# Performance work log

Measured on AMD Instinct MI355X. Metric: run time of the kernel, lower is better.

Reference implementation:

```python
import jax, jax.numpy as jnp
import numpy as np

TAPS = 5
DELAY = 3
ITERATIONS = 2
EPS = 1e-10


def _wpe_one_iteration(Y, power):
    # Y: (B, F, C, T) complex64, power: (B, F, T) float32
    B, F, C, T = Y.shape
    inv_p = 1.0 / jnp.clip(power, EPS)
    Tq = T - DELAY - TAPS + 1  # number of valid frames
    # signal_framing(Y, TAPS, 1)[..., :Tq, :] then reverse last dim:
    # Y_tilde[..., t, k] = Y[..., t + TAPS - 1 - k]  -> (B, F, C, Tq, TAPS)
    Y_tilde = jnp.stack(
        [Y[..., TAPS - 1 - k: TAPS - 1 - k + Tq] for k in range(TAPS)], axis=-1)
    Y_tilde_ip = Y_tilde * inv_p[..., None, DELAY + TAPS - 1:, None]
    # correlation matrix (B, F, taps*C, taps*C)
    R = jnp.einsum('bfdtk,bfetl->bfkdle', jnp.conj(Y_tilde_ip), Y_tilde)
    R = R.reshape(B, F, TAPS * C, TAPS * C)
    # correlation vector (B, F, taps, C, C): indices (k, e, d)
    P = jnp.einsum('bfdtk,bfet->bfked', jnp.conj(Y_tilde_ip),
                   Y[..., DELAY + TAPS - 1:])
    # regularize and invert (batched small complex systems)
    R = R + EPS * jnp.eye(TAPS * C, dtype=R.dtype)
    inv_R = jnp.linalg.inv(R)
    # (B,F,k,e,d) -> (B,F,e,k,d) -> (B,F,C,taps*C)
    vec = jnp.transpose(P, (0, 1, 3, 2, 4)).reshape(B, F, C, TAPS * C)
    # stacked = vec @ inv_R^T  -> (B, F, C, taps*C)
    stacked = jnp.einsum('bfck,bflk->bfcl', vec, inv_R)
    # (B,F,C1,taps,C2) -> filter_matrix_conj (B,F,taps,C2,C1)
    G_conj = jnp.transpose(stacked.reshape(B, F, C, TAPS, C), (0, 1, 3, 4, 2))
    # delayed copies of Y: Y_shift[..., p, :, t] = Y[..., t - DELAY - p] (zero-padded)
    Y_shift = jnp.stack(
        [jnp.pad(Y[..., :T - DELAY - p], [(0, 0)] * 3 + [(DELAY + p, 0)])
         for p in range(TAPS)], axis=-3)  # (B, F, taps, C, T)
    reverb_tail = jnp.einsum('bfpde,bfpdt->bfet', G_conj, Y_shift)
    return Y - reverb_tail


def setup_inputs() -> dict:
    key = jax.random.key(0)
    k1, k2, k3 = jax.random.split(key, 3)
    B, T, C, F = 8, 600, 8, 257
    data_real = jax.random.normal(k1, (B, T, C, F), dtype=jnp.float32)
    data_imag = jax.random.normal(k2, (B, T, C, F), dtype=jnp.float32)
    ilens = jax.random.randint(k3, (B,), 300, T + 1)
    return {"data_real": data_real, "data_imag": data_imag, "ilens": ilens}


def reference(data_real, data_imag, ilens):
    # data: (B, T, C, F) -> (B, F, C, T)
    Y = jax.lax.complex(data_real, data_imag)
    Y = jnp.transpose(Y, (0, 3, 2, 1))
    B, F, C, T = Y.shape
    # use_dnn_mask=False: power averaged over channels -> (B, F, T)
    power = (Y.real ** 2 + Y.imag ** 2).mean(axis=-2)
    enhanced = Y
    for i in range(ITERATIONS):
        if i > 0:
            power = (enhanced.real ** 2 + enhanced.imag ** 2).mean(axis=-2)
        enhanced = _wpe_one_iteration(Y, power)
    # zero out padded frames (make_pad_mask along T)
    tmask = (jnp.arange(T) < ilens[:, None]).astype(enhanced.real.dtype)
    enhanced = enhanced * tmask[:, None, None, :]
    # back to (B, T, C, F)
    enhanced = jnp.transpose(enhanced, (0, 3, 2, 1))
    return enhanced.real, enhanced.imag
```

## Files before the change

### kernel.cpp

```cpp
#include <hip/hip_runtime.h>
#include <hip/hip_bf16.h>

#define Bb 8
#define Tt 600
#define Cc 8
#define Ff 257
#define TAPS 5
#define DELAY 3
#define KC 40
#define NC 48
#define TQ 593
#define TP 602
#define EPSF 1e-10f
#define NTOT (Bb*Tt*Cc*Ff)

__device__ __forceinline__ float2 cmul2(float2 a, float2 b) {
  return make_float2(a.x*b.x - a.y*b.y, a.x*b.y + a.y*b.x);
}

#define CMAC(acc, ax, ay, b)                    \
  acc.x = fmaf(ax, b.x, acc.x);                 \
  acc.x = fmaf(ay, b.y, acc.x);                 \
  acc.y = fmaf(ax, b.y, acc.y);                 \
  acc.y = fmaf(-(ay), b.x, acc.y);

__global__ __launch_bounds__(256) void k_tin(const float* __restrict__ in_re,
                                             const float* __restrict__ in_im,
                                             float2* __restrict__ Yt) {
  __shared__ float2 tile[32][33];
  int f0 = blockIdx.x * 32, t0 = blockIdx.y * 32;
  int b = blockIdx.z >> 3, c = blockIdx.z & 7;
  int tx = threadIdx.x & 31, ty = threadIdx.x >> 5;
#pragma unroll
  for (int ii = 0; ii < 4; ++ii) {
    int t = t0 + ty + 8 * ii, f = f0 + tx;
    if (t < Tt && f < Ff) {
      size_t idx = (((size_t)b * Tt + t) * Cc + c) * Ff + f;
      tile[ty + 8 * ii][tx] = make_float2(in_re[idx], in_im[idx]);
    }
  }
  __syncthreads();
#pragma unroll
  for (int ii = 0; ii < 4; ++ii) {
    int f = f0 + ty + 8 * ii, t = t0 + tx;
    if (f < Ff && t < Tt) {
      size_t o = (((size_t)b * Ff + f) * Cc + c) * Tt + t;
      Yt[o] = tile[tx][ty + 8 * ii];
    }
  }
}

__global__ __launch_bounds__(512, 4) void k_wpe(const float2* __restrict__ Yt,
                                                float2* __restrict__ enh,
                                                const float* __restrict__ in_re,
                                                const float* __restrict__ in_im,
                                                const int* __restrict__ ilens,
                                                float* __restrict__ out_re,
                                                float* __restrict__ out_im,
                                                int load_direct, int store_direct) {
  __shared__ float2 Yl[Cc][TP];
  __shared__ float2 RP[KC][NC + 1];
  __shared__ float wl[Tt];

  int bf = blockIdx.x;
  int b = bf / Ff, f = bf % Ff;
  int tid = threadIdx.x;
  int half = tid >> 8;
  int stid = tid & 255;
  int ty = stid >> 4, tx = stid & 15;

  if (!load_direct) {
    const float4* Yg = (const float4*)(Yt + (size_t)bf * (Cc * Tt));
    for (int i = tid; i < Cc * Tt / 2; i += 512) {
      float4 v = Yg[i];
      int c = i / (Tt / 2), t2 = (i % (Tt / 2)) * 2;
      *(float4*)&Yl[c][t2] = v;
    }
  } else {
    for (int i = tid; i < Cc * Tt; i += 512) {
      int c = i / Tt, t = i % Tt;
      size_t idx = (((size_t)b * Tt + t) * Cc + c) * Ff + f;
      Yl[c][t] = make_float2(in_re[idx], in_im[idx]);
    }
  }
  __syncthreads();

  const float2* YlF = &Yl[0][0];

  bool rv2 = (ty < 8);
  int roff[3];
#pragma unroll
  for (int a = 0; a < 3; ++a) {
    int r = ty + 16 * a;
    if (a == 2 && !rv2) r = 0;
    int k = r >> 3, d = r & 7;
    roff[a] = d * TP + 4 - k;
  }
  int coff[3];
#pragma unroll
  for (int bb = 0; bb < 3; ++bb) {
    int cc = tx + 16 * bb;
    if (cc < KC) { int k = cc >> 3, d = cc & 7; coff[bb] = d * TP + 4 - k; }
    else         { int e = cc - KC;             coff[bb] = e * TP + 7; }
  }

  int tA = half ? 297 : 0;
  int tB = half ? TQ : 297;

  for (int iter = 0; iter < 3; ++iter) {
    if (iter == 0) {
      for (int t = tid; t < Tt; t += 512) {
        float s = 0.f;
#pragma unroll
        for (int c = 0; c < Cc; ++c) { float2 y = Yl[c][t]; s += y.x*y.x + y.y*y.y; }
        wl[t] = 1.0f / fmaxf(s * 0.125f, EPSF);
      }
    } else {
      for (int t = tid; t < Tt; t += 512) {
        float2 acc[Cc];
#pragma unroll
        for (int e = 0; e < Cc; ++e) acc[e] = Yl[e][t];
        for (int p = 0; p < TAPS; ++p) {
          int ts = t - DELAY - p;
          if (ts < 0) break;
#pragma unroll
          for (int d = 0; d < Cc; ++d) {
            float2 u = Yl[d][ts];
            int j = p * Cc + d;
#pragma unroll
            for (int e = 0; e < Cc; ++e) {
              float2 g = RP[j][KC + e];
              acc[e].x -= g.x*u.x - g.y*u.y;
              acc[e].y -= g.x*u.y + g.y*u.x;
            }
          }
        }
        if (iter == 1) {
          float s = 0.f;
#pragma unroll
          for (int e = 0; e < Cc; ++e) s += acc[e].x*acc[e].x + acc[e].y*acc[e].y;
          wl[t] = 1.0f / fmaxf(s * 0.125f, EPSF);
        } else {
          if (!store_direct) {
            float2* Eg = enh + (size_t)bf * (Cc * Tt);
#pragma unroll
            for (int e = 0; e < Cc; ++e) Eg[e * Tt + t] = acc[e];
          } else {
            int il = ilens[b];
            bool live = (t < il);
#pragma unroll
            for (int e = 0; e < Cc; ++e) {
              float2 v = live ? acc[e] : make_float2(0.f, 0.f);
              size_t idx = (((size_t)b * Tt + t) * Cc + e) * Ff + f;
              out_re[idx] = v.x;
              out_im[idx] = v.y;
            }
          }
        }
      }
    }
    if (iter == 2) break;
    __syncthreads();

    float2 racc[3][3];
#pragma unroll
    for (int a = 0; a < 3; ++a)
#pragma unroll
      for (int bb = 0; bb < 3; ++bb) racc[a][bb] = make_float2(0.f, 0.f);

#pragma unroll 2
    for (int t = tA; t < tB; ++t) {
      float w = wl[t + DELAY + TAPS - 1];
      float2 bv0 = YlF[coff[0] + t];
      float2 bv1 = YlF[coff[1] + t];
      float2 bv2 = YlF[coff[2] + t];
      float2 y0 = YlF[roff[0] + t];
      float2 y1 = YlF[roff[1] + t];
      float a0x = w * y0.x, a0y = w * y0.y;
      float a1x = w * y1.x, a1y = w * y1.y;
      CMAC(racc[0][0], a0x, a0y, bv0);
      CMAC(racc[0][1], a0x, a0y, bv1);
      CMAC(racc[0][2], a0x, a0y, bv2);
      CMAC(racc[1][0], a1x, a1y, bv0);
      CMAC(racc[1][1], a1x, a1y, bv1);
      CMAC(racc[1][2], a1x, a1y, bv2);
      if (rv2) {
        float2 y2 = YlF[roff[2] + t];
        float a2x = w * y2.x, a2y = w * y2.y;
        CMAC(racc[2][0], a2x, a2y, bv0);
        CMAC(racc[2][1], a2x, a2y, bv1);
        CMAC(racc[2][2], a2x, a2y, bv2);
      }
    }

    if (half == 0) {
#pragma unroll
      for (int a = 0; a < 3; ++a) {
        if (a == 2 && !rv2) continue;
        int r = ty + 16 * a;
#pragma unroll
        for (int bb = 0; bb < 3; ++bb) RP[r][tx + 16 * bb] = racc[a][bb];
      }
    }
    __syncthreads();
    if (half == 1) {
#pragma unroll
      for (int a = 0; a < 3; ++a) {
        if (a == 2 && !rv2) continue;
        int r = ty + 16 * a;
#pragma unroll
        for (int bb = 0; bb < 3; ++bb) {
          float2 v = RP[r][tx + 16 * bb];
          v.x += racc[a][bb].x; v.y += racc[a][bb].y;
          RP[r][tx + 16 * bb] = v;
        }
      }
    }
    __syncthreads();

    if (tid < KC) RP[tid][tid].x += EPSF;
    __syncthreads();

    for (int j = 0; j < KC; ++j) {
      float2 pv = RP[j][j];
      float idn = 1.0f / (pv.x*pv.x + pv.y*pv.y);
      float2 ip = make_float2(pv.x * idn, -pv.y * idn);
      for (int k = j + 1 + tid; k < NC; k += 512)
        RP[j][k] = cmul2(RP[j][k], ip);
      __syncthreads();
      int ncols = NC - 1 - j;
      int tot = (KC - 1) * ncols;
      for (int idx = tid; idx < tot; idx += 512) {
        int i = idx / ncols;
        if (i >= j) ++i;
        int k = j + 1 + idx % ncols;
        float2 lij = RP[i][j];
        float2 s = cmul2(lij, RP[j][k]);
        RP[i][k].x -= s.x;
        RP[i][k].y -= s.y;
      }
      __syncthreads();
    }
  }
}

__global__ __launch_bounds__(256) void k_tout(const float2* __restrict__ enh,
                                              const int* __restrict__ ilens,
                                              float* __restrict__ out_re,
                                              float* __restrict__ out_im) {
  __shared__ float2 tile[32][33];
  int t0 = blockIdx.x * 32, f0 = blockIdx.y * 32;
  int b = blockIdx.z >> 3, c = blockIdx.z & 7;
  int tx = threadIdx.x & 31, ty = threadIdx.x >> 5;
#pragma unroll
  for (int ii = 0; ii < 4; ++ii) {
    int f = f0 + ty + 8 * ii, t = t0 + tx;
    if (f < Ff && t < Tt)
      tile[ty + 8 * ii][tx] = enh[(((size_t)b * Ff + f) * Cc + c) * Tt + t];
  }
  __syncthreads();
  int il = ilens[b];
#pragma unroll
  for (int ii = 0; ii < 4; ++ii) {
    int t = t0 + ty + 8 * ii, f = f0 + tx;
    if (t < Tt && f < Ff) {
      float2 v = tile[tx][ty + 8 * ii];
      if (t >= il) v = make_float2(0.f, 0.f);
      size_t idx = (((size_t)b * Tt + t) * Cc + c) * Ff + f;
      out_re[idx] = v.x;
      out_im[idx] = v.y;
    }
  }
}

extern "C" void kernel_launch(void* const* d_in, const int* in_sizes, int n_in,
                              void* d_out, int out_size, void* d_ws, size_t ws_size,
                              hipStream_t stream) {
  const float* in_re = (const float*)d_in[0];
  const float* in_im = (const float*)d_in[1];
  const int* ilens = (const int*)d_in[2];
  float* out_re = (float*)d_out;
  float* out_im = out_re + NTOT;

  size_t ybytes = (size_t)Bb * Ff * Cc * Tt * sizeof(float2);
  int have_yt  = ws_size >= ybytes;
  int have_enh = ws_size >= 2 * ybytes;
  float2* Yt  = (float2*)d_ws;
  float2* enh = (float2*)((char*)d_ws + ybytes);

  if (have_yt) {
    dim3 g((Ff + 31) / 32, (Tt + 31) / 32, Bb * Cc);
    k_tin<<<g, dim3(256), 0, stream>>>(in_re, in_im, Yt);
  }
  {
    dim3 g(Bb * Ff);
    k_wpe<<<g, dim3(512), 0, stream>>>(Yt, enh, in_re, in_im, ilens,
                                       out_re, out_im,
                                       have_yt ? 0 : 1, have_enh ? 0 : 1);
  }
  if (have_enh) {
    dim3 g((Tt + 31) / 32, (Ff + 31) / 32, Bb * Cc);
    k_tout<<<g, dim3(256), 0, stream>>>(enh, ilens, out_re, out_im);
  }
}
```

Measured before the change: 1.267 ms.

## Restructure correlation accumulation to per-channel-pair threads with sliding tap window

The R/P correlation accumulation is remapped so each thread owns one (d,e) channel pair and accumulates all 5x5 tap combinations plus the 5 P entries in registers. A rotating 5-element register window reuses shifted Y samples across taps instead of reloading them from LDS, which cuts shared-memory traffic per FMA. Time is split across 8 wave groups instead of 2 halves, and the partial sums are reduced serially through shared memory over 8 synchronized passes. The cost is heavier register pressure (about 60 float2 accumulators) under launch bounds of 512 threads with 4 blocks, plus the extra reduction barriers.

```diff
diff --git a/kernel.cpp b/kernel.cpp
--- a/kernel.cpp
+++ b/kernel.cpp
@@ -9,6 +9,7 @@
 #define DELAY 3
 #define KC 40
 #define NC 48
+#define RPW 52
 #define TQ 593
 #define TP 602
 #define EPSF 1e-10f
@@ -49,6 +50,27 @@
     }
   }
 }
+
+#define ABODY(u) do {                                                     \
+  float2 ynd = Yd[tb + (u) + 4];                                          \
+  float2 yne = Ye[tb + (u) + 4];                                          \
+  float2 yep = Ye[tb + (u) + 7];                                          \
+  float w = wl[tb + (u) + 7];                                             \
+  wd[((u)+4)%5] = ynd; we[((u)+4)%5] = yne;                               \
+  float ax[5], ay[5];                                                     \
+  _Pragma("unroll")                                                       \
+  for (int k = 0; k < 5; ++k) {                                           \
+    float2 yr = wd[((u)+4-k)%5]; ax[k] = w*yr.x; ay[k] = w*yr.y;          \
+  }                                                                       \
+  _Pragma("unroll")                                                       \
+  for (int l = 0; l < 5; ++l) {                                           \
+    float2 yc = we[((u)+4-l)%5];                                          \
+    _Pragma("unroll")                                                     \
+    for (int k = 0; k < 5; ++k) { CMAC(rac[k][l], ax[k], ay[k], yc); }    \
+  }                                                                       \
+  _Pragma("unroll")                                                       \
+  for (int k = 0; k < 5; ++k) { CMAC(pac[k], ax[k], ay[k], yep); }        \
+} while (0)
 
 __global__ __launch_bounds__(512, 4) void k_wpe(const float2* __restrict__ Yt,
                                                 float2* __restrict__ enh,
@@ -59,15 +81,16 @@
                                                 float* __restrict__ out_im,
                                                 int load_direct, int store_direct) {
   __shared__ float2 Yl[Cc][TP];
-  __shared__ float2 RP[KC][NC + 1];
+  __shared__ float2 RP[KC][RPW];
   __shared__ float wl[Tt];
 
   int bf = blockIdx.x;
   int b = bf / Ff, f = bf % Ff;
   int tid = threadIdx.x;
-  int half = tid >> 8;
-  int stid = tid & 255;
-  int ty = stid >> 4, tx = stid & 15;
+  int group = tid >> 6;
+  int lane = tid & 63;
+  int d = lane & 7;
+  int e = lane >> 3;
 
   if (!load_direct) {
     const float4* Yg = (const float4*)(Yt + (size_t)bf * (Cc * Tt));
@@ -85,27 +108,11 @@
   }
   __syncthreads();
 
-  const float2* YlF = &Yl[0][0];
-
-  bool rv2 = (ty < 8);
-  int roff[3];
-#pragma unroll
-  for (int a = 0; a < 3; ++a) {
-    int r = ty + 16 * a;
-    if (a == 2 && !rv2) r = 0;
-    int k = r >> 3, d = r & 7;
-    roff[a] = d * TP + 4 - k;
-  }
-  int coff[3];
-#pragma unroll
-  for (int bb = 0; bb < 3; ++bb) {
-    int cc = tx + 16 * bb;
-    if (cc < KC) { int k = cc >> 3, d = cc & 7; coff[bb] = d * TP + 4 - k; }
-    else         { int e = cc - KC;             coff[bb] = e * TP + 7; }
-  }
-
-  int tA = half ? 297 : 0;
-  int tB = half ? TQ : 297;
+  const float2* Yd = &Yl[d][0];
+  const float2* Ye = &Yl[e][0];
+
+  int tA = (TQ * group) >> 3;
+  int tB = (TQ * (group + 1)) >> 3;
 
   for (int iter = 0; iter < 3; ++iter) {
     if (iter == 0) {
@@ -119,39 +126,39 @@
       for (int t = tid; t < Tt; t += 512) {
         float2 acc[Cc];
 #pragma unroll
-        for (int e = 0; e < Cc; ++e) acc[e] = Yl[e][t];
+        for (int ee = 0; ee < Cc; ++ee) acc[ee] = Yl[ee][t];
         for (int p = 0; p < TAPS; ++p) {
           int ts = t - DELAY - p;
           if (ts < 0) break;
 #pragma unroll
-          for (int d = 0; d < Cc; ++d) {
-            float2 u = Yl[d][ts];
-            int j = p * Cc + d;
-#pragma unroll
-            for (int e = 0; e < Cc; ++e) {
-              float2 g = RP[j][KC + e];
-              acc[e].x -= g.x*u.x - g.y*u.y;
-              acc[e].y -= g.x*u.y + g.y*u.x;
+          for (int dd = 0; dd < Cc; ++dd) {
+            float2 u = Yl[dd][ts];
+            int j = p * Cc + dd;
+#pragma unroll
+            for (int ee = 0; ee < Cc; ++ee) {
+              float2 g = RP[j][KC + ee];
+              acc[ee].x -= g.x*u.x - g.y*u.y;
+              acc[ee].y -= g.x*u.y + g.y*u.x;
             }
           }
         }
         if (iter == 1) {
           float s = 0.f;
 #pragma unroll
-          for (int e = 0; e < Cc; ++e) s += acc[e].x*acc[e].x + acc[e].y*acc[e].y;
+          for (int ee = 0; ee < Cc; ++ee) s += acc[ee].x*acc[ee].x + acc[ee].y*acc[ee].y;
           wl[t] = 1.0f / fmaxf(s * 0.125f, EPSF);
         } else {
           if (!store_direct) {
             float2* Eg = enh + (size_t)bf * (Cc * Tt);
 #pragma unroll
-            for (int e = 0; e < Cc; ++e) Eg[e * Tt + t] = acc[e];
+            for (int ee = 0; ee < Cc; ++ee) Eg[ee * Tt + t] = acc[ee];
           } else {
             int il = ilens[b];
             bool live = (t < il);
 #pragma unroll
-            for (int e = 0; e < Cc; ++e) {
-              float2 v = live ? acc[e] : make_float2(0.f, 0.f);
-              size_t idx = (((size_t)b * Tt + t) * Cc + e) * Ff + f;
+            for (int ee = 0; ee < Cc; ++ee) {
+              float2 v = live ? acc[ee] : make_float2(0.f, 0.f);
+              size_t idx = (((size_t)b * Tt + t) * Cc + ee) * Ff + f;
               out_re[idx] = v.x;
               out_im[idx] = v.y;
             }
@@ -162,61 +169,66 @@
     if (iter == 2) break;
     __syncthreads();
 
-    float2 racc[3][3];
-#pragma unroll
-    for (int a = 0; a < 3; ++a)
-#pragma unroll
-      for (int bb = 0; bb < 3; ++bb) racc[a][bb] = make_float2(0.f, 0.f);
-
-#pragma unroll 2
-    for (int t = tA; t < tB; ++t) {
-      float w = wl[t + DELAY + TAPS - 1];
-      float2 bv0 = YlF[coff[0] + t];
-      float2 bv1 = YlF[coff[1] + t];
-      float2 bv2 = YlF[coff[2] + t];
-      float2 y0 = YlF[roff[0] + t];
-      float2 y1 = YlF[roff[1] + t];
-      float a0x = w * y0.x, a0y = w * y0.y;
-      float a1x = w * y1.x, a1y = w * y1.y;
-      CMAC(racc[0][0], a0x, a0y, bv0);
-      CMAC(racc[0][1], a0x, a0y, bv1);
-      CMAC(racc[0][2], a0x, a0y, bv2);
-      CMAC(racc[1][0], a1x, a1y, bv0);
-      CMAC(racc[1][1], a1x, a1y, bv1);
-      CMAC(racc[1][2], a1x, a1y, bv2);
-      if (rv2) {
-        float2 y2 = YlF[roff[2] + t];
-        float a2x = w * y2.x, a2y = w * y2.y;
-        CMAC(racc[2][0], a2x, a2y, bv0);
-        CMAC(racc[2][1], a2x, a2y, bv1);
-        CMAC(racc[2][2], a2x, a2y, bv2);
-      }
-    }
-
-    if (half == 0) {
-#pragma unroll
-      for (int a = 0; a < 3; ++a) {
-        if (a == 2 && !rv2) continue;
-        int r = ty + 16 * a;
-#pragma unroll
-        for (int bb = 0; bb < 3; ++bb) RP[r][tx + 16 * bb] = racc[a][bb];
-      }
-    }
-    __syncthreads();
-    if (half == 1) {
-#pragma unroll
-      for (int a = 0; a < 3; ++a) {
-        if (a == 2 && !rv2) continue;
-        int r = ty + 16 * a;
-#pragma unroll
-        for (int bb = 0; bb < 3; ++bb) {
-          float2 v = RP[r][tx + 16 * bb];
-          v.x += racc[a][bb].x; v.y += racc[a][bb].y;
-          RP[r][tx + 16 * bb] = v;
+    float2 rac[5][5], pac[5];
+#pragma unroll
+    for (int k = 0; k < 5; ++k) {
+#pragma unroll
+      for (int l = 0; l < 5; ++l) rac[k][l] = make_float2(0.f, 0.f);
+      pac[k] = make_float2(0.f, 0.f);
+    }
+
+    float2 wd[5], we[5];
+#pragma unroll
+    for (int i = 0; i < 4; ++i) { wd[i] = Yd[tA + i]; we[i] = Ye[tA + i]; }
+
+    int tb = tA;
+    for (; tb + 5 <= tB; tb += 5) {
+      ABODY(0); ABODY(1); ABODY(2); ABODY(3); ABODY(4);
+    }
+    for (int t = tb; t < tB; ++t) {
+      float2 yep = Ye[t + 7];
+      float w = wl[t + 7];
+      float ax[5], ay[5];
+#pragma unroll
+      for (int k = 0; k < 5; ++k) {
+        float2 yr = Yd[t + 4 - k]; ax[k] = w*yr.x; ay[k] = w*yr.y;
+      }
+#pragma unroll
+      for (int l = 0; l < 5; ++l) {
+        float2 yc = Ye[t + 4 - l];
+#pragma unroll
+        for (int k = 0; k < 5; ++k) { CMAC(rac[k][l], ax[k], ay[k], yc); }
+      }
+#pragma unroll
+      for (int k = 0; k < 5; ++k) { CMAC(pac[k], ax[k], ay[k], yep); }
+    }
+
+    for (int gpass = 0; gpass < 8; ++gpass) {
+      if (group == gpass) {
+        if (gpass == 0) {
+#pragma unroll
+          for (int k = 0; k < 5; ++k) {
+#pragma unroll
+            for (int l = 0; l < 5; ++l) RP[k*8+d][l*8+e] = rac[k][l];
+            RP[k*8+d][KC+e] = pac[k];
+          }
+        } else {
+#pragma unroll
+          for (int k = 0; k < 5; ++k) {
+#pragma unroll
+            for (int l = 0; l < 5; ++l) {
+              float2 v = RP[k*8+d][l*8+e];
+              v.x += rac[k][l].x; v.y += rac[k][l].y;
+              RP[k*8+d][l*8+e] = v;
+            }
+            float2 v = RP[k*8+d][KC+e];
+            v.x += pac[k].x; v.y += pac[k].y;
+            RP[k*8+d][KC+e] = v;
+          }
         }
       }
-    }
-    __syncthreads();
+      __syncthreads();
+    }
 
     if (tid < KC) RP[tid][tid].x += EPSF;
     __syncthreads();
```

New measurement: 1.203 ms. -5.0%, faster.
